# Performance work log

Measured on AMD Instinct MI355X. Metric: run time of the kernel, lower is better.

Reference implementation:

```python
import jax, jax.numpy as jnp
import numpy as np

D_MODEL = 1024
NUM_HEADS = 16
D_K = D_MODEL // NUM_HEADS


def setup_inputs() -> dict:
    key = jax.random.key(0)
    ks = jax.random.split(key, 11)
    B, S = 2, 2048
    scale = 1.0 / np.sqrt(D_MODEL)
    inp = {
        "Q": jax.random.normal(ks[0], (B, S, D_MODEL), jnp.float32),
        "K": jax.random.normal(ks[1], (B, S, D_MODEL), jnp.float32),
        "V": jax.random.normal(ks[2], (B, S, D_MODEL), jnp.float32),
        # per-head projection weights stacked on head axis: [H, d_model, d_k]
        "Wq": jax.random.uniform(ks[3], (NUM_HEADS, D_MODEL, D_K), jnp.float32, -scale, scale),
        "bq": jax.random.uniform(ks[4], (NUM_HEADS, D_K), jnp.float32, -scale, scale),
        "Wk": jax.random.uniform(ks[5], (NUM_HEADS, D_MODEL, D_K), jnp.float32, -scale, scale),
        "bk": jax.random.uniform(ks[6], (NUM_HEADS, D_K), jnp.float32, -scale, scale),
        "Wv": jax.random.uniform(ks[7], (NUM_HEADS, D_MODEL, D_K), jnp.float32, -scale, scale),
        "bv": jax.random.uniform(ks[8], (NUM_HEADS, D_K), jnp.float32, -scale, scale),
        "Wo": jax.random.uniform(ks[9], (D_MODEL, D_MODEL), jnp.float32, -scale, scale),
        "bo": jax.random.uniform(ks[10], (D_MODEL,), jnp.float32, -scale, scale),
    }
    return inp


def reference(Q, K, V, Wq, bq, Wk, bk, Wv, bv, Wo, bo):
    # Batched equivalent of the per-head loop: project all heads at once.
    q = jnp.einsum("bsd,hdk->bhsk", Q, Wq) + bq[None, :, None, :]
    k = jnp.einsum("bsd,hdk->bhsk", K, Wk) + bk[None, :, None, :]
    v = jnp.einsum("bsd,hdk->bhsk", V, Wv) + bv[None, :, None, :]
    scores = jnp.einsum("bhqk,bhmk->bhqm", q, k) / jnp.sqrt(jnp.float32(D_K))
    weights = jax.nn.softmax(scores, axis=-1)
    attn = jnp.einsum("bhqm,bhmk->bhqk", weights, v)  # [B,H,S,d_k]
    B, H, S, Dk = attn.shape
    concat = attn.transpose(0, 2, 1, 3).reshape(B, S, H * Dk)  # head-order concat
    return concat @ Wo.T + bo
```

## Files before the change

### kernel.cpp

```cpp
#include <hip/hip_runtime.h>
#include <math.h>

#define BATCH 2
#define SLEN 2048
#define DM 1024
#define NH 16
#define DK 64
#define STILES (SLEN / 64)

typedef __attribute__((ext_vector_type(8))) __bf16 bf16x8;
typedef __attribute__((ext_vector_type(4))) float f32x4;

__device__ __forceinline__ unsigned short f2bf(float x) {
  unsigned u = __builtin_bit_cast(unsigned, x);
  unsigned r = (u + 0x7fffu + ((u >> 16) & 1u)) >> 16;
  return (unsigned short)r;
}
__device__ __forceinline__ void splitbf(float x, unsigned short& h,
                                        unsigned short& l) {
  unsigned u = __builtin_bit_cast(unsigned, x);
  h = (unsigned short)(u >> 16);
  float hf = __builtin_bit_cast(float, u & 0xffff0000u);
  l = (unsigned short)(__builtin_bit_cast(unsigned, x - hf) >> 16);
}

__device__ __forceinline__ void gld16(const unsigned short* g,
                                      unsigned short* l) {
  __builtin_amdgcn_global_load_lds(
      (const __attribute__((address_space(1))) void*)g,
      (__attribute__((address_space(3))) void*)l, 16, 0, 0);
}

__global__ __launch_bounds__(256)
void convert_w(const float* __restrict__ Wq, const float* __restrict__ Wk,
               const float* __restrict__ Wv, unsigned short* __restrict__ Wqt,
               unsigned short* __restrict__ Wkt,
               unsigned short* __restrict__ Wvt) {
  const int kb = blockIdx.x, h = blockIdx.y, z = blockIdx.z;
  const float* W = (z == 0 ? Wq : z == 1 ? Wk : Wv) +
                   ((size_t)h * DM + kb * 64) * DK;
  unsigned short* D = (z == 0 ? Wqt : z == 1 ? Wkt : Wvt);

  __shared__ float T[64][65];
  const int tid = threadIdx.x;
  {
    int r = tid >> 2, c0 = (tid & 3) * 16;
#pragma unroll
    for (int i = 0; i < 4; ++i) {
      float4 f = *(const float4*)(W + (size_t)r * DK + c0 + i * 4);
      T[r][c0 + i * 4 + 0] = f.x;
      T[r][c0 + i * 4 + 1] = f.y;
      T[r][c0 + i * 4 + 2] = f.z;
      T[r][c0 + i * 4 + 3] = f.w;
    }
  }
  __syncthreads();
  int j = tid >> 2, p = tid & 3;
  int n = h * 64 + j;
  int kloc = p * 16;
  unsigned short hi[16], lo[16];
#pragma unroll
  for (int i = 0; i < 16; ++i) splitbf(T[kloc + i][j], hi[i], lo[i]);
  int kglob = kb * 64 + kloc;
  int blk = kglob >> 5;
  int c0 = (kglob & 31) >> 3;
  int key = n & 7;
  unsigned short* rowp = D + (size_t)n * 2048 + blk * 64;
  uint4 u0, u1;
  u0.x = (unsigned)hi[0] | ((unsigned)hi[1] << 16);
  u0.y = (unsigned)hi[2] | ((unsigned)hi[3] << 16);
  u0.z = (unsigned)hi[4] | ((unsigned)hi[5] << 16);
  u0.w = (unsigned)hi[6] | ((unsigned)hi[7] << 16);
  u1.x = (unsigned)hi[8] | ((unsigned)hi[9] << 16);
  u1.y = (unsigned)hi[10] | ((unsigned)hi[11] << 16);
  u1.z = (unsigned)hi[12] | ((unsigned)hi[13] << 16);
  u1.w = (unsigned)hi[14] | ((unsigned)hi[15] << 16);
  *(uint4*)(rowp + ((c0 ^ key)) * 8) = u0;
  *(uint4*)(rowp + (((c0 + 1) ^ key)) * 8) = u1;
  u0.x = (unsigned)lo[0] | ((unsigned)lo[1] << 16);
  u0.y = (unsigned)lo[2] | ((unsigned)lo[3] << 16);
  u0.z = (unsigned)lo[4] | ((unsigned)lo[5] << 16);
  u0.w = (unsigned)lo[6] | ((unsigned)lo[7] << 16);
  u1.x = (unsigned)lo[8] | ((unsigned)lo[9] << 16);
  u1.y = (unsigned)lo[10] | ((unsigned)lo[11] << 16);
  u1.z = (unsigned)lo[12] | ((unsigned)lo[13] << 16);
  u1.w = (unsigned)lo[14] | ((unsigned)lo[15] << 16);
  *(uint4*)(rowp + (((c0 + 4) ^ key)) * 8) = u0;
  *(uint4*)(rowp + (((c0 + 5) ^ key)) * 8) = u1;
}

__global__ __launch_bounds__(256)
void convert_x(const float* __restrict__ Q, const float* __restrict__ K,
               const float* __restrict__ V, unsigned short* __restrict__ Xp) {
  const int m = blockIdx.x, z = blockIdx.y;
  const float* src = (z == 0 ? Q : z == 1 ? K : V) + (size_t)m * DM;
  unsigned short* dst =
      Xp + (size_t)z * (8u * 1024 * 1024) + (size_t)m * 2048;
  const int k0 = threadIdx.x * 4;
  float4 f = *(const float4*)(src + k0);
  ushort4 h4, l4;
  splitbf(f.x, h4.x, l4.x);
  splitbf(f.y, h4.y, l4.y);
  splitbf(f.z, h4.z, l4.z);
  splitbf(f.w, h4.w, l4.w);
  int blk = k0 >> 5, ch = (k0 & 31) >> 3, off = k0 & 7, key = m & 7;
  unsigned short* rowp = dst + blk * 64;
  *(ushort4*)(rowp + ((ch ^ key)) * 8 + off) = h4;
  *(ushort4*)(rowp + (((ch + 4) ^ key)) * 8 + off) = l4;
}

__global__ __launch_bounds__(256)
void convert_wo(const float* __restrict__ Wo, unsigned short* __restrict__ Wot) {
  const int n = blockIdx.x;
  const int t = threadIdx.x;
  const int k0 = t * 4;
  float4 f = *(const float4*)(Wo + (size_t)n * DM + k0);
  ushort4 h4, l4;
  splitbf(f.x, h4.x, l4.x);
  splitbf(f.y, h4.y, l4.y);
  splitbf(f.z, h4.z, l4.z);
  splitbf(f.w, h4.w, l4.w);
  int blk = k0 >> 5, ch = (k0 & 31) >> 3, off = k0 & 7, key = n & 7;
  unsigned short* rowp = Wot + (size_t)n * 2048 + blk * 64;
  *(ushort4*)(rowp + ((ch ^ key)) * 8 + off) = h4;
  *(ushort4*)(rowp + (((ch + 4) ^ key)) * 8 + off) = l4;
}

__global__ __launch_bounds__(512, 2)
void proj_gemm(const unsigned short* __restrict__ Xp,
               const unsigned short* __restrict__ Wqt,
               const unsigned short* __restrict__ Wkt,
               const unsigned short* __restrict__ Wvt,
               const float* __restrict__ bq, const float* __restrict__ bk,
               const float* __restrict__ bv, unsigned short* __restrict__ q_all,
               unsigned short* __restrict__ k_all,
               unsigned short* __restrict__ vt) {
  const int ntile = blockIdx.x, mt = blockIdx.y, z = blockIdx.z;
  const unsigned short* Bw = (z == 0 ? Wqt : z == 1 ? Wkt : Wvt);
  const float* bias = (z == 0 ? bq : z == 1 ? bk : bv);

  __shared__ alignas(16) unsigned short As[2][256 * 64];
  __shared__ alignas(16) unsigned short Bs[2][256 * 64];

  const int tid = threadIdx.x;
  const int lane = tid & 63, w = tid >> 6;
  const int l15 = lane & 15, quad = lane >> 4;
  const int wm = (w >> 2) * 128, wn = (w & 3) * 64;
  const int kx = l15 & 7;
  const int r0 = tid >> 3, seg = tid & 7;

  const unsigned short* Ap =
      Xp + (size_t)z * (8u * 1024 * 1024) + (size_t)(mt * 256) * 2048;
  const unsigned short* Bp = Bw + (size_t)(ntile * 256) * 2048;

#define STAGE_A(bf, hh, t)                                                    \
  do {                                                                        \
    const unsigned short* _s =                                                \
        Ap + (size_t)((hh)*64 + r0) * 2048 + (t)*64 + seg * 8;                \
    unsigned short* _d = &As[bf][((hh)*64 + r0) * 64 + seg * 8];              \
    gld16(_s, _d);                                                            \
    gld16(_s + (size_t)128 * 2048, _d + 128 * 64);                            \
  } while (0)
#define STAGE_B(bf, hh, t)                                                    \
  do {                                                                        \
    int _rb = ((r0 >> 5) << 6) + (hh)*32 + (r0 & 31);                         \
    const unsigned short* _s = Bp + (size_t)_rb * 2048 + (t)*64 + seg * 8;    \
    unsigned short* _d = &Bs[bf][_rb * 64 + seg * 8];                         \
    gld16(_s, _d);                                                            \
    gld16(_s + (size_t)128 * 2048, _d + 128 * 64);                            \
  } while (0)
#define VMW(n) asm volatile("s_waitcnt vmcnt(" #n ")" ::: "memory")

#define PHASE(BUF, QM, QN, STG, VMS)                                          \
  do {                                                                        \
    bf16x8 ah_[4], al_[4], bh_[2], bl_[2];                                    \
    _Pragma("unroll") for (int i_ = 0; i_ < 4; ++i_) {                        \
      const unsigned short* p_ =                                              \
          &As[BUF][(wm + (QM)*64 + i_ * 16 + l15) * 64];                      \
      ah_[i_] = *(const bf16x8*)(p_ + ((quad ^ kx)) * 8);                     \
      al_[i_] = *(const bf16x8*)(p_ + (((quad + 4) ^ kx)) * 8);               \
    }                                                                         \
    _Pragma("unroll") for (int j_ = 0; j_ < 2; ++j_) {                        \
      const unsigned short* p_ =                                              \
          &Bs[BUF][(wn + (QN)*32 + j_ * 16 + l15) * 64];                      \
      bh_[j_] = *(const bf16x8*)(p_ + ((quad ^ kx)) * 8);                     \
      bl_[j_] = *(const bf16x8*)(p_ + (((quad + 4) ^ kx)) * 8);               \
    }                                                                         \
    STG;                                                                      \
    VMS;                                                                      \
    asm volatile("s_waitcnt lgkmcnt(8)" ::: "memory");                        \
    __builtin_amdgcn_s_barrier();                                             \
    asm volatile("s_waitcnt lgkmcnt(0)" ::: "memory");                        \
    __builtin_amdgcn_sched_barrier(0);                                        \
    __builtin_amdgcn_s_setprio(1);                                            \
    _Pragma("unroll") for (int j_ = 0; j_ < 2; ++j_)                          \
        _Pragma("unroll") for (int i_ = 0; i_ < 4; ++i_) {                    \
      acc[QM][QN][i_][j_] = __builtin_amdgcn_mfma_f32_16x16x32_bf16(          \
          ah_[i_], bh_[j_], acc[QM][QN][i_][j_], 0, 0, 0);                    \
      acc[QM][QN][i_][j_] = __builtin_amdgcn_mfma_f32_16x16x32_bf16(          \
          al_[i_], bh_[j_], acc[QM][QN][i_][j_], 0, 0, 0);                    \
      acc[QM][QN][i_][j_] = __builtin_amdgcn_mfma_f32_16x16x32_bf16(          \
          ah_[i_], bl_[j_], acc[QM][QN][i_][j_], 0, 0, 0);                    \
    }                                                                         \
    __builtin_amdgcn_s_setprio(0);                                            \
    __builtin_amdgcn_sched_barrier(0);                                        \
    __builtin_amdgcn_s_barrier();                                             \
  } while (0)

  f32x4 acc[2][2][4][2];
#pragma unroll
  for (int a0 = 0; a0 < 2; ++a0)
#pragma unroll
    for (int a1 = 0; a1 < 2; ++a1)
#pragma unroll
      for (int a2 = 0; a2 < 4; ++a2)
#pragma unroll
        for (int a3 = 0; a3 < 2; ++a3)
          acc[a0][a1][a2][a3] = (f32x4){0.f, 0.f, 0.f, 0.f};

  STAGE_B(0, 0, 0);
  STAGE_A(0, 0, 0);
  STAGE_A(0, 1, 0);
  STAGE_B(0, 1, 0);
  STAGE_B(1, 0, 1);
  STAGE_A(1, 0, 1);
  VMW(4);
  __builtin_amdgcn_s_barrier();

#pragma unroll 1
  for (int it2 = 0; it2 < 16; ++it2) {
    const int O = 2 * it2 + 1;
    const int En = 2 * it2 + 2;
    const int On = 2 * it2 + 3;
    const bool sE = (it2 < 15);
    PHASE(0, 0, 0, STAGE_A(1, 1, O), (void)0);
    PHASE(0, 1, 0, STAGE_B(1, 1, O), (void)0);
    PHASE(0, 0, 1, if (sE) STAGE_B(0, 0, En), (void)0);
    PHASE(0, 1, 1, if (sE) STAGE_A(0, 0, En),
          if (sE) { VMW(4); } else { VMW(0); });
    PHASE(1, 0, 0, if (sE) STAGE_A(0, 1, En), (void)0);
    PHASE(1, 1, 0, if (sE) STAGE_B(0, 1, En), (void)0);
    PHASE(1, 0, 1, if (sE) STAGE_B(1, 0, On), (void)0);
    PHASE(1, 1, 1, if (sE) STAGE_A(1, 0, On), if (sE) VMW(4));
  }
#undef PHASE
#undef VMW
#undef STAGE_A
#undef STAGE_B

  if (z <= 1) {
    unsigned short* dst = (z == 0 ? q_all : k_all);
#pragma unroll
    for (int qm = 0; qm < 2; ++qm)
#pragma unroll
      for (int qn = 0; qn < 2; ++qn)
#pragma unroll
        for (int i = 0; i < 4; ++i)
#pragma unroll
          for (int j = 0; j < 2; ++j) {
            int n = ntile * 256 + wn + qn * 32 + j * 16 + l15;
            int hh_ = n >> 6, d = n & 63;
            int chi = (d >> 5) * 8 + ((d & 31) >> 3);
            float bn = bias[n];
#pragma unroll
            for (int r = 0; r < 4; ++r) {
              int m = mt * 256 + wm + qm * 64 + i * 16 + quad * 4 + r;
              int key = m & 15;
              size_t rb = (size_t)m * 2048 + hh_ * 128;
              unsigned short hv, lv;
              splitbf(acc[qm][qn][i][j][r] + bn, hv, lv);
              dst[rb + ((chi ^ key)) * 8 + (d & 7)] = hv;
              dst[rb + (((chi + 4) ^ key)) * 8 + (d & 7)] = lv;
            }
          }
  } else {
#pragma unroll
    for (int qm = 0; qm < 2; ++qm)
#pragma unroll
      for (int qn = 0; qn < 2; ++qn)
#pragma unroll
        for (int i = 0; i < 4; ++i)
#pragma unroll
          for (int j = 0; j < 2; ++j) {
            int n = ntile * 256 + wn + qn * 32 + j * 16 + l15;
            int h = n >> 6, d = n & 63;
            float bn = bias[n];
            int m0 = mt * 256 + wm + qm * 64 + i * 16 + quad * 4;
            int b = m0 >> 11, s0_ = m0 & 2047;
            int kt = s0_ >> 6, sl = s0_ & 63;
            int ch = sl >> 3, off = sl & 7, key = d & 15;
            ushort4 h4, l4;
            splitbf(acc[qm][qn][i][j][0] + bn, h4.x, l4.x);
            splitbf(acc[qm][qn][i][j][1] + bn, h4.y, l4.y);
            splitbf(acc[qm][qn][i][j][2] + bn, h4.z, l4.z);
            splitbf(acc[qm][qn][i][j][3] + bn, h4.w, l4.w);
            size_t base =
                (size_t)(b * NH + h) * 262144 + (size_t)d * 4096 + kt * 128;
            *(ushort4*)(vt + base + ((ch ^ key)) * 8 + off) = h4;
            *(ushort4*)(vt + base + (((ch + 8) ^ key)) * 8 + off) = l4;
          }
  }
}

__global__ __launch_bounds__(256)
void out_gemm(const unsigned short* __restrict__ a_all,
              const unsigned short* __restrict__ Wot,
              const float* __restrict__ bo, float* __restrict__ out) {
  const int ntile = blockIdx.x, mt = blockIdx.y;

  __shared__ alignas(16) unsigned short As[2][64 * 64];
  __shared__ alignas(16) unsigned short Bs[2][128 * 64];

  const int tid = threadIdx.x;
  const int lane = tid & 63, w = tid >> 6;
  const int l15 = lane & 15, quad = lane >> 4;
  const int wn = w * 32;
  const int kx = l15 & 7;

  const unsigned short* Ap = a_all + (size_t)(mt * 64) * 2048;
  const unsigned short* Bp = Wot + (size_t)(ntile * 128) * 2048;

#pragma unroll
  for (int it = 0; it < 2; ++it) {
    int s = tid + it * 256;
    int r = s >> 3, seg = s & 7;
    gld16(Ap + (size_t)r * 2048 + seg * 8, &As[0][s * 8]);
  }
#pragma unroll
  for (int it = 0; it < 4; ++it) {
    int s = tid + it * 256;
    int r = s >> 3, seg = s & 7;
    gld16(Bp + (size_t)r * 2048 + seg * 8, &Bs[0][s * 8]);
  }

  f32x4 acc[4][2];
#pragma unroll
  for (int i = 0; i < 4; ++i)
#pragma unroll
    for (int j = 0; j < 2; ++j) acc[i][j] = (f32x4){0.f, 0.f, 0.f, 0.f};

  int cur = 0;
  for (int kk = 0; kk < 32; ++kk) {
    __syncthreads();

    if (kk + 1 < 32) {
      int blk = (kk + 1) * 64;
#pragma unroll
      for (int it = 0; it < 2; ++it) {
        int s = tid + it * 256;
        int r = s >> 3, seg = s & 7;
        gld16(Ap + (size_t)r * 2048 + blk + seg * 8, &As[cur ^ 1][s * 8]);
      }
#pragma unroll
      for (int it = 0; it < 4; ++it) {
        int s = tid + it * 256;
        int r = s >> 3, seg = s & 7;
        gld16(Bp + (size_t)r * 2048 + blk + seg * 8, &Bs[cur ^ 1][s * 8]);
      }
    }

    bf16x8 ah[4], al[4];
#pragma unroll
    for (int i = 0; i < 4; ++i) {
      const unsigned short* p = &As[cur][(i * 16 + l15) * 64];
      ah[i] = *(const bf16x8*)(p + ((quad ^ kx)) * 8);
      al[i] = *(const bf16x8*)(p + (((quad + 4) ^ kx)) * 8);
    }
#pragma unroll
    for (int j = 0; j < 2; ++j) {
      const unsigned short* p = &Bs[cur][(wn + j * 16 + l15) * 64];
      bf16x8 bh = *(const bf16x8*)(p + ((quad ^ kx)) * 8);
      bf16x8 bl = *(const bf16x8*)(p + (((quad + 4) ^ kx)) * 8);
#pragma unroll
      for (int i = 0; i < 4; ++i) {
        acc[i][j] = __builtin_amdgcn_mfma_f32_16x16x32_bf16(ah[i], bh, acc[i][j], 0, 0, 0);
        acc[i][j] = __builtin_amdgcn_mfma_f32_16x16x32_bf16(al[i], bh, acc[i][j], 0, 0, 0);
        acc[i][j] = __builtin_amdgcn_mfma_f32_16x16x32_bf16(ah[i], bl, acc[i][j], 0, 0, 0);
      }
    }
    cur ^= 1;
  }

#pragma unroll
  for (int i = 0; i < 4; ++i)
#pragma unroll
    for (int j = 0; j < 2; ++j) {
      int n = ntile * 128 + wn + j * 16 + l15;
      float bn = bo[n];
#pragma unroll
      for (int r = 0; r < 4; ++r) {
        int m = mt * 64 + i * 16 + quad * 4 + r;
        out[(size_t)m * DM + n] = acc[i][j][r] + bn;
      }
    }
}

__global__ __launch_bounds__(256)
void attn_kernel(const unsigned short* __restrict__ q_all,
                 const unsigned short* __restrict__ k_all,
                 const unsigned short* __restrict__ vt,
                 unsigned short* __restrict__ a_all) {
  const int qt = blockIdx.x, h = blockIdx.y, b = blockIdx.z;
  const unsigned short* vp = vt + (size_t)(b * NH + h) * 262144;

  __shared__ alignas(16) unsigned short Ks[2][64 * 128];
  __shared__ alignas(16) unsigned short Vs[2][64 * 128];
  __shared__ alignas(16) unsigned short Ps[128 * 64];

  const int tid = threadIdx.x;
  const int lane = tid & 63;
  const int w = tid >> 6;
  const int l15 = lane & 15;
  const int quad = lane >> 4;

  bf16x8 qf[2][2][2];
#pragma unroll
  for (int rt = 0; rt < 2; ++rt) {
    const unsigned short* qrow =
        q_all + (size_t)(b * SLEN + qt * 128 + w * 32 + rt * 16 + l15) * 2048 +
        h * 128;
#pragma unroll
    for (int kb = 0; kb < 2; ++kb) {
      qf[rt][kb][0] = *(const bf16x8*)(qrow + ((kb * 8 + quad) ^ l15) * 8);
      qf[rt][kb][1] = *(const bf16x8*)(qrow + ((kb * 8 + quad + 4) ^ l15) * 8);
    }
  }

  {
    const unsigned short* ksrc = k_all + (size_t)(b * SLEN) * 2048 + h * 128;
#pragma unroll
    for (int it = 0; it < 4; ++it) {
      int ss = it * 256 + tid;
      int r = ss >> 4, p = ss & 15;
      gld16(ksrc + (size_t)r * 2048 + p * 8, &Ks[0][ss * 8]);
    }
#pragma unroll
    for (int it = 0; it < 4; ++it) {
      int ss = it * 256 + tid;
      int d = ss >> 4, p = ss & 15;
      gld16(vp + (size_t)d * 4096 + p * 8, &Vs[0][ss * 8]);
    }
  }

  f32x4 o[2][4];
  float lpart[2];
#pragma unroll
  for (int rt = 0; rt < 2; ++rt) {
    lpart[rt] = 0.f;
#pragma unroll
    for (int nt = 0; nt < 4; ++nt) o[rt][nt] = (f32x4){0.f, 0.f, 0.f, 0.f};
  }

  int cur = 0;
  for (int kt = 0; kt < STILES; ++kt) {
    __syncthreads();

    if (kt + 1 < STILES) {
      const unsigned short* ksrc =
          k_all + (size_t)(b * SLEN + (kt + 1) * 64) * 2048 + h * 128;
#pragma unroll
      for (int it = 0; it < 4; ++it) {
        int ss = it * 256 + tid;
        int r = ss >> 4, p = ss & 15;
        gld16(ksrc + (size_t)r * 2048 + p * 8, &Ks[cur ^ 1][ss * 8]);
      }
#pragma unroll
      for (int it = 0; it < 4; ++it) {
        int ss = it * 256 + tid;
        int d = ss >> 4, p = ss & 15;
        gld16(vp + (size_t)d * 4096 + (kt + 1) * 128 + p * 8,
              &Vs[cur ^ 1][ss * 8]);
      }
    }

    f32x4 sc[2][4];
#pragma unroll
    for (int rt = 0; rt < 2; ++rt)
#pragma unroll
      for (int ct = 0; ct < 4; ++ct) sc[rt][ct] = (f32x4){0.f, 0.f, 0.f, 0.f};
    __builtin_amdgcn_s_setprio(1);
#pragma unroll
    for (int ct = 0; ct < 4; ++ct) {
      const unsigned short* kbase = &Ks[cur][(ct * 16 + l15) * 128];
#pragma unroll
      for (int kb = 0; kb < 2; ++kb) {
        bf16x8 kh = *(const bf16x8*)(kbase + ((kb * 8 + quad) ^ l15) * 8);
        bf16x8 kl = *(const bf16x8*)(kbase + ((kb * 8 + quad + 4) ^ l15) * 8);
#pragma unroll
        for (int rt = 0; rt < 2; ++rt) {
          sc[rt][ct] = __builtin_amdgcn_mfma_f32_16x16x32_bf16(kh, qf[rt][kb][0], sc[rt][ct], 0, 0, 0);
          sc[rt][ct] = __builtin_amdgcn_mfma_f32_16x16x32_bf16(kl, qf[rt][kb][0], sc[rt][ct], 0, 0, 0);
          sc[rt][ct] = __builtin_amdgcn_mfma_f32_16x16x32_bf16(kh, qf[rt][kb][1], sc[rt][ct], 0, 0, 0);
        }
      }
    }
    __builtin_amdgcn_s_setprio(0);

#pragma unroll
    for (int rt = 0; rt < 2; ++rt) {
      const int prow = w * 32 + rt * 16 + l15;
      const int pk = (l15 >> 1) & 7;
      unsigned short* prowp = &Ps[prow * 64 + (quad & 1) * 4];
#pragma unroll
      for (int ct = 0; ct < 4; ++ct) {
        float e0 = __expf(sc[rt][ct][0] * 0.125f);
        float e1 = __expf(sc[rt][ct][1] * 0.125f);
        float e2 = __expf(sc[rt][ct][2] * 0.125f);
        float e3 = __expf(sc[rt][ct][3] * 0.125f);
        lpart[rt] += (e0 + e1) + (e2 + e3);
        unsigned plo, phi;
        asm("v_cvt_pk_bf16_f32 %0, %1, %2" : "=v"(plo) : "v"(e0), "v"(e1));
        asm("v_cvt_pk_bf16_f32 %0, %1, %2" : "=v"(phi) : "v"(e2), "v"(e3));
        uint2 pu;
        pu.x = plo;
        pu.y = phi;
        *(uint2*)(prowp + (((ct * 2 + (quad >> 1)) ^ pk)) * 8) = pu;
      }
    }
    asm volatile("s_waitcnt lgkmcnt(0)" ::: "memory");
    __builtin_amdgcn_sched_barrier(0);

    int rk = (l15 >> 1) & 7;
#pragma unroll
    for (int kb = 0; kb < 2; ++kb) {
      bf16x8 pf[2];
#pragma unroll
      for (int rt = 0; rt < 2; ++rt)
        pf[rt] = *(const bf16x8*)(&Ps[(w * 32 + rt * 16 + l15) * 64 +
                                      (((kb * 4 + quad) ^ rk)) * 8]);
      __builtin_amdgcn_s_setprio(1);
#pragma unroll
      for (int nt = 0; nt < 4; ++nt) {
        const unsigned short* vb = &Vs[cur][(nt * 16 + l15) * 128];
        bf16x8 vh = *(const bf16x8*)(vb + (((kb * 4 + quad) ^ l15)) * 8);
        bf16x8 vl = *(const bf16x8*)(vb + (((kb * 4 + quad + 8) ^ l15)) * 8);
#pragma unroll
        for (int rt = 0; rt < 2; ++rt) {
          o[rt][nt] = __builtin_amdgcn_mfma_f32_16x16x32_bf16(pf[rt], vh, o[rt][nt], 0, 0, 0);
          o[rt][nt] = __builtin_amdgcn_mfma_f32_16x16x32_bf16(pf[rt], vl, o[rt][nt], 0, 0, 0);
        }
      }
      __builtin_amdgcn_s_setprio(0);
    }
    cur ^= 1;
  }

#pragma unroll
  for (int rt = 0; rt < 2; ++rt) {
    float lv = lpart[rt];
    lv += __shfl_xor(lv, 16, 64);
    lv += __shfl_xor(lv, 32, 64);
    float invv = 1.f / lv;
    float inv[4];
#pragma unroll
    for (int r = 0; r < 4; ++r) inv[r] = __shfl(invv, quad * 4 + r, 64);
#pragma unroll
    for (int nt = 0; nt < 4; ++nt) {
      int c = h * 64 + nt * 16 + l15;
      int Bb = c >> 5;
      int d32 = c & 31;
      int ch = d32 >> 3, off = d32 & 7;
#pragma unroll
      for (int r = 0; r < 4; ++r) {
        float val = o[rt][nt][r] * inv[r];
        int srow = qt * 128 + w * 32 + rt * 16 + quad * 4 + r;
        int key = srow & 7;
        size_t g = (size_t)(b * SLEN + srow) * 2048 + Bb * 64;
        unsigned short hv, lv2;
        splitbf(val, hv, lv2);
        a_all[g + ((ch ^ key)) * 8 + off] = hv;
        a_all[g + (((ch + 4) ^ key)) * 8 + off] = lv2;
      }
    }
  }
}

extern "C" void kernel_launch(void* const* d_in, const int* in_sizes, int n_in,
                              void* d_out, int out_size, void* d_ws,
                              size_t ws_size, hipStream_t stream) {
  (void)in_sizes; (void)n_in; (void)out_size; (void)ws_size;
  const float* Q = (const float*)d_in[0];
  const float* K = (const float*)d_in[1];
  const float* V = (const float*)d_in[2];
  const float* Wq = (const float*)d_in[3];
  const float* bq = (const float*)d_in[4];
  const float* Wk = (const float*)d_in[5];
  const float* bk = (const float*)d_in[6];
  const float* Wv = (const float*)d_in[7];
  const float* bv = (const float*)d_in[8];
  const float* Wo = (const float*)d_in[9];
  const float* bo = (const float*)d_in[10];
  float* out = (float*)d_out;

  unsigned short* us = (unsigned short*)d_ws;
  const size_t M8 = 8u * 1024 * 1024;
  unsigned short* q_all = us;
  unsigned short* k_all = us + M8;
  unsigned short* vt = us + 2 * M8;
  unsigned short* a_all = us + 3 * M8;
  unsigned short* Wqt = a_all;
  unsigned short* Wkt = a_all + 2 * 1024 * 1024;
  unsigned short* Wvt = a_all + 4 * 1024 * 1024;
  unsigned short* Xp = us + 4 * M8;
  unsigned short* Wot = q_all;

  convert_w<<<dim3(16, 16, 3), 256, 0, stream>>>(Wq, Wk, Wv, Wqt, Wkt, Wvt);
  convert_x<<<dim3(4096, 3), 256, 0, stream>>>(Q, K, V, Xp);
  proj_gemm<<<dim3(4, 16, 3), 512, 0, stream>>>(Xp, Wqt, Wkt, Wvt, bq, bk, bv,
                                                q_all, k_all, vt);
  attn_kernel<<<dim3(SLEN / 128, NH, BATCH), 256, 0, stream>>>(q_all, k_all,
                                                               vt, a_all);
  convert_wo<<<dim3(1024), 256, 0, stream>>>(Wo, Wot);
  out_gemm<<<dim3(8, 64), 256, 0, stream>>>(a_all, Wot, bo, out);
}
```

Baseline: 339.5 us.

## Merge GEMM phases into four phases each covering both N quadrants

Restructures the projection GEMM main loop from eight phases per iteration to four. Each phase now loads the A fragments once and reuses them for both N sub-tiles, loading the second B fragment set mid-phase. This halves the barriers and the redundant A LDS reads per iteration. Each phase now issues two stage operations, which raises register pressure and changes how global loads are spread between MFMA blocks. The vmcnt wait counts are left unchanged even though more loads are now in flight per phase.

```diff
diff --git a/kernel.cpp b/kernel.cpp
--- a/kernel.cpp
+++ b/kernel.cpp
@@ -171,18 +171,18 @@
   } while (0)
 #define VMW(n) asm volatile("s_waitcnt vmcnt(" #n ")" ::: "memory")
 
-#define PHASE(BUF, QM, QN, STG, VMS)                                          \
+#define PHASE4(BUF, QM, STG, VMS)                                             \
   do {                                                                        \
-    bf16x8 ah_[4], al_[4], bh_[2], bl_[2];                                    \
+    bf16x8 ah_[4], al_[4];                                                    \
     _Pragma("unroll") for (int i_ = 0; i_ < 4; ++i_) {                        \
       const unsigned short* p_ =                                              \
           &As[BUF][(wm + (QM)*64 + i_ * 16 + l15) * 64];                      \
       ah_[i_] = *(const bf16x8*)(p_ + ((quad ^ kx)) * 8);                     \
       al_[i_] = *(const bf16x8*)(p_ + (((quad + 4) ^ kx)) * 8);               \
     }                                                                         \
+    bf16x8 bh_[2], bl_[2];                                                    \
     _Pragma("unroll") for (int j_ = 0; j_ < 2; ++j_) {                        \
-      const unsigned short* p_ =                                              \
-          &Bs[BUF][(wn + (QN)*32 + j_ * 16 + l15) * 64];                      \
+      const unsigned short* p_ = &Bs[BUF][(wn + j_ * 16 + l15) * 64];         \
       bh_[j_] = *(const bf16x8*)(p_ + ((quad ^ kx)) * 8);                     \
       bl_[j_] = *(const bf16x8*)(p_ + (((quad + 4) ^ kx)) * 8);               \
     }                                                                         \
@@ -195,12 +195,30 @@
     __builtin_amdgcn_s_setprio(1);                                            \
     _Pragma("unroll") for (int j_ = 0; j_ < 2; ++j_)                          \
         _Pragma("unroll") for (int i_ = 0; i_ < 4; ++i_) {                    \
-      acc[QM][QN][i_][j_] = __builtin_amdgcn_mfma_f32_16x16x32_bf16(          \
-          ah_[i_], bh_[j_], acc[QM][QN][i_][j_], 0, 0, 0);                    \
-      acc[QM][QN][i_][j_] = __builtin_amdgcn_mfma_f32_16x16x32_bf16(          \
-          al_[i_], bh_[j_], acc[QM][QN][i_][j_], 0, 0, 0);                    \
-      acc[QM][QN][i_][j_] = __builtin_amdgcn_mfma_f32_16x16x32_bf16(          \
-          ah_[i_], bl_[j_], acc[QM][QN][i_][j_], 0, 0, 0);                    \
+      acc[QM][0][i_][j_] = __builtin_amdgcn_mfma_f32_16x16x32_bf16(           \
+          ah_[i_], bh_[j_], acc[QM][0][i_][j_], 0, 0, 0);                     \
+      acc[QM][0][i_][j_] = __builtin_amdgcn_mfma_f32_16x16x32_bf16(           \
+          al_[i_], bh_[j_], acc[QM][0][i_][j_], 0, 0, 0);                     \
+      acc[QM][0][i_][j_] = __builtin_amdgcn_mfma_f32_16x16x32_bf16(           \
+          ah_[i_], bl_[j_], acc[QM][0][i_][j_], 0, 0, 0);                     \
+    }                                                                         \
+    __builtin_amdgcn_sched_barrier(0);                                        \
+    bf16x8 bh2_[2], bl2_[2];                                                  \
+    _Pragma("unroll") for (int j_ = 0; j_ < 2; ++j_) {                        \
+      const unsigned short* p_ = &Bs[BUF][(wn + 32 + j_ * 16 + l15) * 64];    \
+      bh2_[j_] = *(const bf16x8*)(p_ + ((quad ^ kx)) * 8);                    \
+      bl2_[j_] = *(const bf16x8*)(p_ + (((quad + 4) ^ kx)) * 8);              \
+    }                                                                         \
+    asm volatile("s_waitcnt lgkmcnt(0)" ::: "memory");                        \
+    __builtin_amdgcn_sched_barrier(0);                                        \
+    _Pragma("unroll") for (int j_ = 0; j_ < 2; ++j_)                          \
+        _Pragma("unroll") for (int i_ = 0; i_ < 4; ++i_) {                    \
+      acc[QM][1][i_][j_] = __builtin_amdgcn_mfma_f32_16x16x32_bf16(           \
+          ah_[i_], bh2_[j_], acc[QM][1][i_][j_], 0, 0, 0);                    \
+      acc[QM][1][i_][j_] = __builtin_amdgcn_mfma_f32_16x16x32_bf16(           \
+          al_[i_], bh2_[j_], acc[QM][1][i_][j_], 0, 0, 0);                    \
+      acc[QM][1][i_][j_] = __builtin_amdgcn_mfma_f32_16x16x32_bf16(           \
+          ah_[i_], bl2_[j_], acc[QM][1][i_][j_], 0, 0, 0);                    \
     }                                                                         \
     __builtin_amdgcn_s_setprio(0);                                            \
     __builtin_amdgcn_sched_barrier(0);                                        \
@@ -233,17 +251,15 @@
     const int En = 2 * it2 + 2;
     const int On = 2 * it2 + 3;
     const bool sE = (it2 < 15);
-    PHASE(0, 0, 0, STAGE_A(1, 1, O), (void)0);
-    PHASE(0, 1, 0, STAGE_B(1, 1, O), (void)0);
-    PHASE(0, 0, 1, if (sE) STAGE_B(0, 0, En), (void)0);
-    PHASE(0, 1, 1, if (sE) STAGE_A(0, 0, En),
-          if (sE) { VMW(4); } else { VMW(0); });
-    PHASE(1, 0, 0, if (sE) STAGE_A(0, 1, En), (void)0);
-    PHASE(1, 1, 0, if (sE) STAGE_B(0, 1, En), (void)0);
-    PHASE(1, 0, 1, if (sE) STAGE_B(1, 0, On), (void)0);
-    PHASE(1, 1, 1, if (sE) STAGE_A(1, 0, On), if (sE) VMW(4));
-  }
-#undef PHASE
+    PHASE4(0, 0, { STAGE_A(1, 1, O); STAGE_B(1, 1, O); }, (void)0);
+    PHASE4(0, 1,
+           if (sE) { STAGE_B(0, 0, En); STAGE_A(0, 0, En); },
+           if (sE) { VMW(4); } else { VMW(0); });
+    PHASE4(1, 0, if (sE) { STAGE_A(0, 1, En); STAGE_B(0, 1, En); }, (void)0);
+    PHASE4(1, 1, if (sE) { STAGE_B(1, 0, On); STAGE_A(1, 0, On); },
+           if (sE) VMW(4));
+  }
+#undef PHASE4
 #undef VMW
 #undef STAGE_A
 #undef STAGE_B
```

New measurement: 332.9 us. -2.0%, faster.

## Simplify proj_gemm pipeline to per-k-tile double buffering and retile out_gemm

Applied to the files above, without the earlier changes.

proj_gemm drops its eight-phase interleaved staging (half-tile loads spread across MFMA phases) in favour of a plain double buffer. Each k-step now loads the whole next A/B tile and then runs all MFMAs from the current one, with a split lgkmcnt wait between the two M halves. out_gemm moves from 64x128 tiles with 256 threads to 256x64 tiles with 512 threads, with explicit vmcnt waits and priority hints, and launches a 16x16 grid. The aim is fewer barriers and cheaper out_gemm staging, at the cost of less fine-grained load/compute overlap in proj_gemm and a different occupancy profile.

```diff
diff --git a/kernel.cpp b/kernel.cpp
--- a/kernel.cpp
+++ b/kernel.cpp
@@ -147,66 +147,26 @@
   const int l15 = lane & 15, quad = lane >> 4;
   const int wm = (w >> 2) * 128, wn = (w & 3) * 64;
   const int kx = l15 & 7;
-  const int r0 = tid >> 3, seg = tid & 7;
 
   const unsigned short* Ap =
       Xp + (size_t)z * (8u * 1024 * 1024) + (size_t)(mt * 256) * 2048;
   const unsigned short* Bp = Bw + (size_t)(ntile * 256) * 2048;
 
-#define STAGE_A(bf, hh, t)                                                    \
+#define STAGE(bf, t)                                                          \
   do {                                                                        \
-    const unsigned short* _s =                                                \
-        Ap + (size_t)((hh)*64 + r0) * 2048 + (t)*64 + seg * 8;                \
-    unsigned short* _d = &As[bf][((hh)*64 + r0) * 64 + seg * 8];              \
-    gld16(_s, _d);                                                            \
-    gld16(_s + (size_t)128 * 2048, _d + 128 * 64);                            \
-  } while (0)
-#define STAGE_B(bf, hh, t)                                                    \
-  do {                                                                        \
-    int _rb = ((r0 >> 5) << 6) + (hh)*32 + (r0 & 31);                         \
-    const unsigned short* _s = Bp + (size_t)_rb * 2048 + (t)*64 + seg * 8;    \
-    unsigned short* _d = &Bs[bf][_rb * 64 + seg * 8];                         \
-    gld16(_s, _d);                                                            \
-    gld16(_s + (size_t)128 * 2048, _d + 128 * 64);                            \
+    _Pragma("unroll") for (int it_ = 0; it_ < 4; ++it_) {                     \
+      int s_ = tid + it_ * 512;                                               \
+      int r_ = s_ >> 3, sg_ = s_ & 7;                                         \
+      gld16(Ap + (size_t)r_ * 2048 + (t)*64 + sg_ * 8, &As[bf][s_ * 8]);      \
+    }                                                                         \
+    _Pragma("unroll") for (int it_ = 0; it_ < 4; ++it_) {                     \
+      int s_ = tid + it_ * 512;                                               \
+      int r_ = s_ >> 3, sg_ = s_ & 7;                                         \
+      gld16(Bp + (size_t)r_ * 2048 + (t)*64 + sg_ * 8, &Bs[bf][s_ * 8]);      \
+    }                                                                         \
   } while (0)
 #define VMW(n) asm volatile("s_waitcnt vmcnt(" #n ")" ::: "memory")
 
-#define PHASE(BUF, QM, QN, STG, VMS)                                          \
-  do {                                                                        \
-    bf16x8 ah_[4], al_[4], bh_[2], bl_[2];                                    \
-    _Pragma("unroll") for (int i_ = 0; i_ < 4; ++i_) {                        \
-      const unsigned short* p_ =                                              \
-          &As[BUF][(wm + (QM)*64 + i_ * 16 + l15) * 64];                      \
-      ah_[i_] = *(const bf16x8*)(p_ + ((quad ^ kx)) * 8);                     \
-      al_[i_] = *(const bf16x8*)(p_ + (((quad + 4) ^ kx)) * 8);               \
-    }                                                                         \
-    _Pragma("unroll") for (int j_ = 0; j_ < 2; ++j_) {                        \
-      const unsigned short* p_ =                                              \
-          &Bs[BUF][(wn + (QN)*32 + j_ * 16 + l15) * 64];                      \
-      bh_[j_] = *(const bf16x8*)(p_ + ((quad ^ kx)) * 8);                     \
-      bl_[j_] = *(const bf16x8*)(p_ + (((quad + 4) ^ kx)) * 8);               \
-    }                                                                         \
-    STG;                                                                      \
-    VMS;                                                                      \
-    asm volatile("s_waitcnt lgkmcnt(8)" ::: "memory");                        \
-    __builtin_amdgcn_s_barrier();                                             \
-    asm volatile("s_waitcnt lgkmcnt(0)" ::: "memory");                        \
-    __builtin_amdgcn_sched_barrier(0);                                        \
-    __builtin_amdgcn_s_setprio(1);                                            \
-    _Pragma("unroll") for (int j_ = 0; j_ < 2; ++j_)                          \
-        _Pragma("unroll") for (int i_ = 0; i_ < 4; ++i_) {                    \
-      acc[QM][QN][i_][j_] = __builtin_amdgcn_mfma_f32_16x16x32_bf16(          \
-          ah_[i_], bh_[j_], acc[QM][QN][i_][j_], 0, 0, 0);                    \
-      acc[QM][QN][i_][j_] = __builtin_amdgcn_mfma_f32_16x16x32_bf16(          \
-          al_[i_], bh_[j_], acc[QM][QN][i_][j_], 0, 0, 0);                    \
-      acc[QM][QN][i_][j_] = __builtin_amdgcn_mfma_f32_16x16x32_bf16(          \
-          ah_[i_], bl_[j_], acc[QM][QN][i_][j_], 0, 0, 0);                    \
-    }                                                                         \
-    __builtin_amdgcn_s_setprio(0);                                            \
-    __builtin_amdgcn_sched_barrier(0);                                        \
-    __builtin_amdgcn_s_barrier();                                             \
-  } while (0)
-
   f32x4 acc[2][2][4][2];
 #pragma unroll
   for (int a0 = 0; a0 < 2; ++a0)
@@ -218,35 +178,81 @@
         for (int a3 = 0; a3 < 2; ++a3)
           acc[a0][a1][a2][a3] = (f32x4){0.f, 0.f, 0.f, 0.f};
 
-  STAGE_B(0, 0, 0);
-  STAGE_A(0, 0, 0);
-  STAGE_A(0, 1, 0);
-  STAGE_B(0, 1, 0);
-  STAGE_B(1, 0, 1);
-  STAGE_A(1, 0, 1);
-  VMW(4);
-  __builtin_amdgcn_s_barrier();
+  STAGE(0, 0);
 
 #pragma unroll 1
-  for (int it2 = 0; it2 < 16; ++it2) {
-    const int O = 2 * it2 + 1;
-    const int En = 2 * it2 + 2;
-    const int On = 2 * it2 + 3;
-    const bool sE = (it2 < 15);
-    PHASE(0, 0, 0, STAGE_A(1, 1, O), (void)0);
-    PHASE(0, 1, 0, STAGE_B(1, 1, O), (void)0);
-    PHASE(0, 0, 1, if (sE) STAGE_B(0, 0, En), (void)0);
-    PHASE(0, 1, 1, if (sE) STAGE_A(0, 0, En),
-          if (sE) { VMW(4); } else { VMW(0); });
-    PHASE(1, 0, 0, if (sE) STAGE_A(0, 1, En), (void)0);
-    PHASE(1, 1, 0, if (sE) STAGE_B(0, 1, En), (void)0);
-    PHASE(1, 0, 1, if (sE) STAGE_B(1, 0, On), (void)0);
-    PHASE(1, 1, 1, if (sE) STAGE_A(1, 0, On), if (sE) VMW(4));
-  }
-#undef PHASE
+  for (int t = 0; t < 32; ++t) {
+    const int buf = t & 1;
+    if (t + 1 < 32) {
+      STAGE(buf ^ 1, t + 1);
+      VMW(8);
+    } else {
+      VMW(0);
+    }
+    __builtin_amdgcn_s_barrier();
+
+    bf16x8 bh[2][2], bl[2][2];
+#pragma unroll
+    for (int qn = 0; qn < 2; ++qn)
+#pragma unroll
+      for (int j = 0; j < 2; ++j) {
+        const unsigned short* p = &Bs[buf][(wn + qn * 32 + j * 16 + l15) * 64];
+        bh[qn][j] = *(const bf16x8*)(p + ((quad ^ kx)) * 8);
+        bl[qn][j] = *(const bf16x8*)(p + (((quad + 4) ^ kx)) * 8);
+      }
+    bf16x8 ah[4], al[4];
+#pragma unroll
+    for (int i = 0; i < 4; ++i) {
+      const unsigned short* p = &As[buf][(wm + i * 16 + l15) * 64];
+      ah[i] = *(const bf16x8*)(p + ((quad ^ kx)) * 8);
+      al[i] = *(const bf16x8*)(p + (((quad + 4) ^ kx)) * 8);
+    }
+    bf16x8 ah1[4], al1[4];
+#pragma unroll
+    for (int i = 0; i < 4; ++i) {
+      const unsigned short* p = &As[buf][(wm + 64 + i * 16 + l15) * 64];
+      ah1[i] = *(const bf16x8*)(p + ((quad ^ kx)) * 8);
+      al1[i] = *(const bf16x8*)(p + (((quad + 4) ^ kx)) * 8);
+    }
+    asm volatile("s_waitcnt lgkmcnt(8)" ::: "memory");
+    __builtin_amdgcn_sched_barrier(0);
+    __builtin_amdgcn_s_setprio(1);
+#pragma unroll
+    for (int qn = 0; qn < 2; ++qn)
+#pragma unroll
+      for (int j = 0; j < 2; ++j)
+#pragma unroll
+        for (int i = 0; i < 4; ++i) {
+          acc[0][qn][i][j] = __builtin_amdgcn_mfma_f32_16x16x32_bf16(
+              ah[i], bh[qn][j], acc[0][qn][i][j], 0, 0, 0);
+          acc[0][qn][i][j] = __builtin_amdgcn_mfma_f32_16x16x32_bf16(
+              al[i], bh[qn][j], acc[0][qn][i][j], 0, 0, 0);
+          acc[0][qn][i][j] = __builtin_amdgcn_mfma_f32_16x16x32_bf16(
+              ah[i], bl[qn][j], acc[0][qn][i][j], 0, 0, 0);
+        }
+    __builtin_amdgcn_s_setprio(0);
+    asm volatile("s_waitcnt lgkmcnt(0)" ::: "memory");
+    __builtin_amdgcn_sched_barrier(0);
+    __builtin_amdgcn_s_setprio(1);
+#pragma unroll
+    for (int qn = 0; qn < 2; ++qn)
+#pragma unroll
+      for (int j = 0; j < 2; ++j)
+#pragma unroll
+        for (int i = 0; i < 4; ++i) {
+          acc[1][qn][i][j] = __builtin_amdgcn_mfma_f32_16x16x32_bf16(
+              ah1[i], bh[qn][j], acc[1][qn][i][j], 0, 0, 0);
+          acc[1][qn][i][j] = __builtin_amdgcn_mfma_f32_16x16x32_bf16(
+              al1[i], bh[qn][j], acc[1][qn][i][j], 0, 0, 0);
+          acc[1][qn][i][j] = __builtin_amdgcn_mfma_f32_16x16x32_bf16(
+              ah1[i], bl[qn][j], acc[1][qn][i][j], 0, 0, 0);
+        }
+    __builtin_amdgcn_s_setprio(0);
+    __builtin_amdgcn_sched_barrier(0);
+    __builtin_amdgcn_s_barrier();
+  }
 #undef VMW
-#undef STAGE_A
-#undef STAGE_B
+#undef STAGE
 
   if (z <= 1) {
     unsigned short* dst = (z == 0 ? q_all : k_all);
@@ -302,36 +308,38 @@
   }
 }
 
-__global__ __launch_bounds__(256)
+__global__ __launch_bounds__(512, 2)
 void out_gemm(const unsigned short* __restrict__ a_all,
               const unsigned short* __restrict__ Wot,
               const float* __restrict__ bo, float* __restrict__ out) {
   const int ntile = blockIdx.x, mt = blockIdx.y;
 
-  __shared__ alignas(16) unsigned short As[2][64 * 64];
-  __shared__ alignas(16) unsigned short Bs[2][128 * 64];
+  __shared__ alignas(16) unsigned short As[2][256 * 64];
+  __shared__ alignas(16) unsigned short Bs[2][64 * 64];
 
   const int tid = threadIdx.x;
   const int lane = tid & 63, w = tid >> 6;
   const int l15 = lane & 15, quad = lane >> 4;
-  const int wn = w * 32;
+  const int wm = (w >> 1) * 64, wn = (w & 1) * 32;
   const int kx = l15 & 7;
 
-  const unsigned short* Ap = a_all + (size_t)(mt * 64) * 2048;
-  const unsigned short* Bp = Wot + (size_t)(ntile * 128) * 2048;
-
-#pragma unroll
-  for (int it = 0; it < 2; ++it) {
-    int s = tid + it * 256;
-    int r = s >> 3, seg = s & 7;
-    gld16(Ap + (size_t)r * 2048 + seg * 8, &As[0][s * 8]);
-  }
-#pragma unroll
-  for (int it = 0; it < 4; ++it) {
-    int s = tid + it * 256;
-    int r = s >> 3, seg = s & 7;
-    gld16(Bp + (size_t)r * 2048 + seg * 8, &Bs[0][s * 8]);
-  }
+  const unsigned short* Ap = a_all + (size_t)(mt * 256) * 2048;
+  const unsigned short* Bp = Wot + (size_t)(ntile * 64) * 2048;
+
+#define STAGEO(bf, t)                                                         \
+  do {                                                                        \
+    _Pragma("unroll") for (int it_ = 0; it_ < 4; ++it_) {                     \
+      int s_ = tid + it_ * 512;                                               \
+      int r_ = s_ >> 3, sg_ = s_ & 7;                                         \
+      gld16(Ap + (size_t)r_ * 2048 + (t)*64 + sg_ * 8, &As[bf][s_ * 8]);      \
+    }                                                                         \
+    {                                                                         \
+      int s_ = tid;                                                           \
+      int r_ = s_ >> 3, sg_ = s_ & 7;                                         \
+      gld16(Bp + (size_t)r_ * 2048 + (t)*64 + sg_ * 8, &Bs[bf][s_ * 8]);      \
+    }                                                                         \
+  } while (0)
+#define VMW(n) asm volatile("s_waitcnt vmcnt(" #n ")" ::: "memory")
 
   f32x4 acc[4][2];
 #pragma unroll
@@ -339,57 +347,60 @@
 #pragma unroll
     for (int j = 0; j < 2; ++j) acc[i][j] = (f32x4){0.f, 0.f, 0.f, 0.f};
 
-  int cur = 0;
-  for (int kk = 0; kk < 32; ++kk) {
-    __syncthreads();
-
-    if (kk + 1 < 32) {
-      int blk = (kk + 1) * 64;
-#pragma unroll
-      for (int it = 0; it < 2; ++it) {
-        int s = tid + it * 256;
-        int r = s >> 3, seg = s & 7;
-        gld16(Ap + (size_t)r * 2048 + blk + seg * 8, &As[cur ^ 1][s * 8]);
-      }
-#pragma unroll
-      for (int it = 0; it < 4; ++it) {
-        int s = tid + it * 256;
-        int r = s >> 3, seg = s & 7;
-        gld16(Bp + (size_t)r * 2048 + blk + seg * 8, &Bs[cur ^ 1][s * 8]);
-      }
-    }
-
+  STAGEO(0, 0);
+
+#pragma unroll 1
+  for (int t = 0; t < 32; ++t) {
+    const int buf = t & 1;
+    if (t + 1 < 32) {
+      STAGEO(buf ^ 1, t + 1);
+      VMW(5);
+    } else {
+      VMW(0);
+    }
+    __builtin_amdgcn_s_barrier();
+
+    bf16x8 bh[2], bl[2];
+#pragma unroll
+    for (int j = 0; j < 2; ++j) {
+      const unsigned short* p = &Bs[buf][(wn + j * 16 + l15) * 64];
+      bh[j] = *(const bf16x8*)(p + ((quad ^ kx)) * 8);
+      bl[j] = *(const bf16x8*)(p + (((quad + 4) ^ kx)) * 8);
+    }
     bf16x8 ah[4], al[4];
 #pragma unroll
     for (int i = 0; i < 4; ++i) {
-      const unsigned short* p = &As[cur][(i * 16 + l15) * 64];
+      const unsigned short* p = &As[buf][(wm + i * 16 + l15) * 64];
       ah[i] = *(const bf16x8*)(p + ((quad ^ kx)) * 8);
       al[i] = *(const bf16x8*)(p + (((quad + 4) ^ kx)) * 8);
     }
+    asm volatile("s_waitcnt lgkmcnt(0)" ::: "memory");
+    __builtin_amdgcn_sched_barrier(0);
+    __builtin_amdgcn_s_setprio(1);
+#pragma unroll
+    for (int j = 0; j < 2; ++j)
+#pragma unroll
+      for (int i = 0; i < 4; ++i) {
+        acc[i][j] = __builtin_amdgcn_mfma_f32_16x16x32_bf16(ah[i], bh[j], acc[i][j], 0, 0, 0);
+        acc[i][j] = __builtin_amdgcn_mfma_f32_16x16x32_bf16(al[i], bh[j], acc[i][j], 0, 0, 0);
+        acc[i][j] = __builtin_amdgcn_mfma_f32_16x16x32_bf16(ah[i], bl[j], acc[i][j], 0, 0, 0);
+      }
+    __builtin_amdgcn_s_setprio(0);
+    __builtin_amdgcn_sched_barrier(0);
+    __builtin_amdgcn_s_barrier();
+  }
+#undef VMW
+#undef STAGEO
+
+#pragma unroll
+  for (int i = 0; i < 4; ++i)
 #pragma unroll
     for (int j = 0; j < 2; ++j) {
-      const unsigned short* p = &Bs[cur][(wn + j * 16 + l15) * 64];
-      bf16x8 bh = *(const bf16x8*)(p + ((quad ^ kx)) * 8);
-      bf16x8 bl = *(const bf16x8*)(p + (((quad + 4) ^ kx)) * 8);
-#pragma unroll
-      for (int i = 0; i < 4; ++i) {
-        acc[i][j] = __builtin_amdgcn_mfma_f32_16x16x32_bf16(ah[i], bh, acc[i][j], 0, 0, 0);
-        acc[i][j] = __builtin_amdgcn_mfma_f32_16x16x32_bf16(al[i], bh, acc[i][j], 0, 0, 0);
-        acc[i][j] = __builtin_amdgcn_mfma_f32_16x16x32_bf16(ah[i], bl, acc[i][j], 0, 0, 0);
-      }
-    }
-    cur ^= 1;
-  }
-
-#pragma unroll
-  for (int i = 0; i < 4; ++i)
-#pragma unroll
-    for (int j = 0; j < 2; ++j) {
-      int n = ntile * 128 + wn + j * 16 + l15;
+      int n = ntile * 64 + wn + j * 16 + l15;
       float bn = bo[n];
 #pragma unroll
       for (int r = 0; r < 4; ++r) {
-        int m = mt * 64 + i * 16 + quad * 4 + r;
+        int m = mt * 256 + wm + i * 16 + quad * 4 + r;
         out[(size_t)m * DM + n] = acc[i][j][r] + bn;
       }
     }
@@ -611,5 +622,5 @@
   attn_kernel<<<dim3(SLEN / 128, NH, BATCH), 256, 0, stream>>>(q_all, k_all,
                                                                vt, a_all);
   convert_wo<<<dim3(1024), 256, 0, stream>>>(Wo, Wot);
-  out_gemm<<<dim3(8, 64), 256, 0, stream>>>(a_all, Wot, bo, out);
-}
+  out_gemm<<<dim3(16, 16), 512, 0, stream>>>(a_all, Wot, bo, out);
+}
```

Result: no change. 335.4 us (-1.2%).
